# Optimization experiments

Measured on AMD Instinct MI355X. Metric: run time of the kernel, lower is better.

Reference implementation:

```python
import jax, jax.numpy as jnp
import numpy as np

N_NODES = 50000
N_EDGES = 800000
N_GRAPHS = 64
PIP = 3
N_CLASSES = 10
EPS = 1e-5


def setup_inputs() -> dict:
    key = jax.random.key(0)
    ks = jax.random.split(key, 32)
    s = 0.05
    d = {}
    d["node_feats"] = jax.random.normal(ks[0], (N_NODES, 128), jnp.float32)
    d["edge_w"] = jax.random.uniform(ks[1], (N_EDGES,), jnp.float32)
    # stacked per-branch params
    d["conv_w"] = jax.random.normal(ks[2], (PIP, 96, 128, 3), jnp.float32) * s
    d["conv_b"] = jax.random.normal(ks[3], (PIP, 96), jnp.float32) * s
    d["gcn_w"] = jax.random.normal(ks[4], (PIP, 96, 54), jnp.float32) * s
    d["gcn_b"] = jax.random.normal(ks[5], (PIP, 54), jnp.float32) * s
    d["bn1_g"] = jnp.ones((96,), jnp.float32)
    d["bn1_b"] = jnp.zeros((96,), jnp.float32)
    d["bn2_g"] = jnp.ones((54,), jnp.float32)
    d["bn2_b"] = jnp.zeros((54,), jnp.float32)
    d["bn3_g"] = jnp.ones((75,), jnp.float32)
    d["bn3_b"] = jnp.zeros((75,), jnp.float32)
    d["press_w"] = jax.random.normal(ks[6], (1, PIP, PIP), jnp.float32) * s
    d["press_b"] = jax.random.normal(ks[7], (1,), jnp.float32) * s
    d["jk_w1"] = jax.random.normal(ks[8], (54, 34), jnp.float32) * s
    d["jk_b1"] = jax.random.normal(ks[9], (34,), jnp.float32) * s
    d["jk_w2"] = jax.random.normal(ks[10], (34, 25), jnp.float32) * s
    d["jk_b2"] = jax.random.normal(ks[11], (25,), jnp.float32) * s
    d["jk_w3"] = jax.random.normal(ks[12], (25, 16), jnp.float32) * s
    d["jk_b3"] = jax.random.normal(ks[13], (16,), jnp.float32) * s
    d["cls1_w"] = jax.random.normal(ks[14], (75, 120), jnp.float32) * s
    d["cls1_b"] = jax.random.normal(ks[15], (120,), jnp.float32) * s
    d["cls2_w"] = jax.random.normal(ks[16], (120, N_CLASSES), jnp.float32) * s
    d["cls2_b"] = jax.random.normal(ks[17], (N_CLASSES,), jnp.float32) * s
    d["edge_src"] = jax.random.randint(ks[18], (N_EDGES,), 0, N_NODES)
    d["edge_dst"] = jax.random.randint(ks[19], (N_EDGES,), 0, N_NODES)
    d["graph_ids"] = jnp.sort(jax.random.randint(ks[20], (N_NODES,), 0, N_GRAPHS))
    return d


def _bn(x, g, b):
    # training-mode BatchNorm1d over axis 0
    m = x.mean(0)
    v = x.var(0)
    return g * (x - m) * jax.lax.rsqrt(v + EPS) + b


def _gconv(h, W, b, src, dst, ew, n):
    # DGL GraphConv norm='none': sum_{(u,v)} w_e * h[u] -> @W + b
    msg = h[src] * ew[:, None]              # [E, F]
    agg = jax.ops.segment_sum(msg, dst, num_segments=n)  # [N, F]
    return agg @ W + b


def _dconv1d(x, w, b, dil):
    # x: [1, Cin, N], w: [Cout, Cin, K]; 'same' length via pad=dil for K=3
    out = jax.lax.conv_general_dilated(
        x, w, window_strides=(1,), padding=[(dil, dil)],
        rhs_dilation=(dil,), dimension_numbers=('NCH', 'OIH', 'NCH'))
    return out + b[None, :, None]


def reference(node_feats, edge_w, conv_w, conv_b, gcn_w, gcn_b,
              bn1_g, bn1_b, bn2_g, bn2_b, bn3_g, bn3_b,
              press_w, press_b, jk_w1, jk_b1, jk_w2, jk_b2, jk_w3, jk_b3,
              cls1_w, cls1_b, cls2_w, cls2_b,
              edge_src, edge_dst, graph_ids):
    n = node_feats.shape[0]
    relu = jax.nn.relu
    # ---- BN_embedding ----
    h0 = node_feats.T[None]                # [1, 128, N]
    h0x = [_dconv1d(h0, conv_w[i], conv_b[i], i + 1) for i in range(PIP)]
    h2x = []
    for i in range(PIP):
        a = h0x[i % PIP][0].T              # [N, 96]
        c = h0x[(i + 1) % PIP][0].T        # [N, 96]
        h1 = _bn(relu(a) + c, bn1_g, bn1_b)          # cross_connect
        t = _gconv(h1, gcn_w[i], gcn_b[i], edge_src, edge_dst, edge_w, n)
        h2x.append(relu(t))                # [N, 54]
    stacked = jnp.stack(h2x, axis=1)       # [N, PIP, 54]
    pressed = jax.lax.conv_general_dilated(
        stacked, press_w, window_strides=(1,), padding='SAME',
        dimension_numbers=('NCH', 'OIH', 'NCH')) + press_b[None, :, None]
    emd_h = _bn(pressed[:, 0, :], bn2_g, bn2_b)      # [N, 54] (dropout = identity, eval)
    # ---- Presentation (JK readout) ----
    h1 = relu(_gconv(emd_h, jk_w1, jk_b1, edge_src, edge_dst, edge_w, n))
    h2 = relu(_gconv(h1, jk_w2, jk_b2, edge_src, edge_dst, edge_w, n))
    h3 = relu(_gconv(h2, jk_w3, jk_b3, edge_src, edge_dst, edge_w, n))
    ac_h = jnp.concatenate([h1, h2, h3], axis=1)     # [N, 75]
    hg = jax.ops.segment_sum(ac_h, graph_ids, num_segments=N_GRAPHS)  # [B, 75]
    logits = _bn(hg, bn3_g, bn3_b) @ cls1_w + cls1_b
    logits = logits @ cls2_w + cls2_b
    return (logits, emd_h)
```

## Files before the change

### kernel.cpp

```cpp
#include <hip/hip_runtime.h>
#include <hip/hip_bf16.h>

#define NND 50000
#define NED 800000
#define NGR 64
#define EPSV 1e-5f
#define NSTR (NND + 8)

__global__ void hist_kernel(const int* __restrict__ dst, int* __restrict__ cnt)
{
    int e = blockIdx.x * 256 + threadIdx.x;
    if (e < NED) atomicAdd(&cnt[dst[e]], 1);
}

__global__ void scanA_kernel(const int* __restrict__ cnt, int* __restrict__ bsum)
{
    __shared__ int buf[256];
    int t = threadIdx.x, base = blockIdx.x * 1024;
    int s = 0;
    for (int i = t; i < 1024; i += 256) {
        int idx = base + i;
        s += (idx < NND) ? cnt[idx] : 0;
    }
    buf[t] = s; __syncthreads();
    for (int off = 128; off; off >>= 1) {
        if (t < off) buf[t] += buf[t + off];
        __syncthreads();
    }
    if (t == 0) bsum[blockIdx.x] = buf[0];
}

__global__ void scanB_kernel(int* __restrict__ bsum, int* __restrict__ rowptr, int nb)
{
    if (threadIdx.x == 0) {
        int acc = 0;
        for (int i = 0; i < nb; i++) { int v = bsum[i]; bsum[i] = acc; acc += v; }
        rowptr[NND] = acc;
    }
}

__global__ void scanC_kernel(const int* __restrict__ cnt, const int* __restrict__ bsum,
                             int* __restrict__ rowptr, int* __restrict__ cursor)
{
    __shared__ int buf[1024];
    int t = threadIdx.x, idx = blockIdx.x * 1024 + t;
    int v = (idx < NND) ? cnt[idx] : 0;
    buf[t] = v; __syncthreads();
    for (int off = 1; off < 1024; off <<= 1) {
        int x = (t >= off) ? buf[t - off] : 0;
        __syncthreads();
        buf[t] += x;
        __syncthreads();
    }
    if (idx < NND) {
        int excl = buf[t] - v + bsum[blockIdx.x];
        rowptr[idx] = excl; cursor[idx] = excl;
    }
}

__global__ void fill_kernel(const int* __restrict__ src, const int* __restrict__ dst,
                            const float* __restrict__ ew, int* __restrict__ cursor,
                            int* __restrict__ csrs, float* __restrict__ csrw)
{
    int e = blockIdx.x * 256 + threadIdx.x;
    if (e < NED) {
        int pos = atomicAdd(&cursor[dst[e]], 1);
        csrs[pos] = src[e];
        csrw[pos] = ew[e];
    }
}

__global__ void grstart_kernel(const int* __restrict__ gid, int* __restrict__ gr)
{
    int t = threadIdx.x;
    if (t > NGR) return;
    if (t == NGR) { gr[NGR] = NND; return; }
    int lo = 0, hi = NND;
    while (lo < hi) { int mid = (lo + hi) >> 1; if (gid[mid] < t) lo = mid + 1; else hi = mid; }
    gr[t] = lo;
}

__global__ void transpose_kernel(const float* __restrict__ nf, float* __restrict__ nfT)
{
    __shared__ float tile[32][33];
    int tx = threadIdx.x & 31, ty = threadIdx.x >> 5;
    int p0 = blockIdx.x * 32, c0 = blockIdx.y * 32;
#pragma unroll
    for (int i = 0; i < 4; i++) {
        int p = p0 + ty + i * 8;
        if (p < NND) tile[ty + i * 8][tx] = nf[(size_t)p * 128 + c0 + tx];
    }
    __syncthreads();
#pragma unroll
    for (int i = 0; i < 4; i++) {
        int c = c0 + ty + i * 8;
        int p = p0 + tx;
        if (p < NND) nfT[(size_t)c * NSTR + 4 + p] = tile[tx][ty + i * 8];
    }
}

__global__ void pad_kernel(float* __restrict__ nfT)
{
    int t = threadIdx.x;
    int c = t >> 3, i = t & 7;
    size_t off = (size_t)c * NSTR + (i < 4 ? i : (NND + i));
    nfT[off] = 0.f;
}

template <int D>
__device__ __forceinline__ void conv_tap4(const float4& lo, const float4& mi, const float4& hi,
                                          const float* __restrict__ wl, int c,
                                          float (&acc)[4][4])
{
    float f0[4], f1[4], f2[4];
    f1[0] = mi.x; f1[1] = mi.y; f1[2] = mi.z; f1[3] = mi.w;
    if (D == 1) {
        f0[0] = lo.w; f0[1] = mi.x; f0[2] = mi.y; f0[3] = mi.z;
        f2[0] = mi.y; f2[1] = mi.z; f2[2] = mi.w; f2[3] = hi.x;
    } else if (D == 2) {
        f0[0] = lo.z; f0[1] = lo.w; f0[2] = mi.x; f0[3] = mi.y;
        f2[0] = mi.z; f2[1] = mi.w; f2[2] = hi.x; f2[3] = hi.y;
    } else {
        f0[0] = lo.y; f0[1] = lo.z; f0[2] = lo.w; f0[3] = mi.x;
        f2[0] = mi.w; f2[1] = hi.x; f2[2] = hi.y; f2[3] = hi.z;
    }
    const int BR = D - 1;
    const float4 a0 = *(const float4*)&wl[((BR * 3 + 0) * 128 + c) * 4];
    const float4 a1 = *(const float4*)&wl[((BR * 3 + 1) * 128 + c) * 4];
    const float4 a2 = *(const float4*)&wl[((BR * 3 + 2) * 128 + c) * 4];
#pragma unroll
    for (int i = 0; i < 4; i++) {
        acc[0][i] += f0[i] * a0.x + f1[i] * a1.x + f2[i] * a2.x;
        acc[1][i] += f0[i] * a0.y + f1[i] * a1.y + f2[i] * a2.y;
        acc[2][i] += f0[i] * a0.z + f1[i] * a1.z + f2[i] * a2.z;
        acc[3][i] += f0[i] * a0.w + f1[i] * a1.w + f2[i] * a2.w;
    }
}

__global__ __launch_bounds__(256)
void conv_y_stats_kernel(const float* __restrict__ nfT, const float* __restrict__ cw,
                         const float* __restrict__ cb, float* __restrict__ Y,
                         float* __restrict__ st1)
{
    __shared__ __align__(16) float wl[3 * 3 * 128 * 4];
    const int t  = threadIdx.x;
    const int og = blockIdx.x;
    for (int l = t; l < 3 * 3 * 128 * 4; l += 256) {
        int j = l & 3; int c = (l >> 2) & 127; int kb = l >> 9;
        int k = kb % 3, br = kb / 3;
        wl[l] = cw[(((size_t)br * 96 + og * 4 + j) * 128 + c) * 3 + k];
    }
    __syncthreads();
    const int pq = blockIdx.y * 1024 + t * 4;
    float acc[3][4][4];
#pragma unroll
    for (int br = 0; br < 3; br++)
#pragma unroll
        for (int j = 0; j < 4; j++) {
            float b = cb[br * 96 + og * 4 + j];
#pragma unroll
            for (int i = 0; i < 4; i++) acc[br][j][i] = b;
        }
    for (int c = 0; c < 128; c++) {
        const float* col = nfT + (size_t)c * NSTR + 4;
        float4 lo = *(const float4*)(col + pq - 4);
        float4 mi = *(const float4*)(col + pq);
        float4 hi = *(const float4*)(col + pq + 4);
        conv_tap4<1>(lo, mi, hi, wl, c, acc[0]);
        conv_tap4<2>(lo, mi, hi, wl, c, acc[1]);
        conv_tap4<3>(lo, mi, hi, wl, c, acc[2]);
    }
#pragma unroll
    for (int j = 0; j < 4; j++)
#pragma unroll
        for (int i = 0; i < 4; i++) {
            float a0 = acc[0][j][i], a1 = acc[1][j][i], a2 = acc[2][j][i];
            acc[0][j][i] = (a0 > 0.f ? a0 : 0.f) + a1;
            acc[1][j][i] = (a1 > 0.f ? a1 : 0.f) + a2;
            acc[2][j][i] = (a2 > 0.f ? a2 : 0.f) + a0;
        }
    bool val[4];
#pragma unroll
    for (int i = 0; i < 4; i++) val[i] = (pq + i) < NND;
    const size_t NM = (size_t)NND * 96;
#pragma unroll
    for (int br = 0; br < 3; br++)
#pragma unroll
        for (int j = 0; j < 4; j++) {
            float s = 0.f, q = 0.f;
#pragma unroll
            for (int i = 0; i < 4; i++)
                if (val[i]) { float v = acc[br][j][i]; s += v; q += v * v; }
            for (int off = 32; off; off >>= 1) {
                s += __shfl_down(s, off, 64);
                q += __shfl_down(q, off, 64);
            }
            if ((t & 63) == 0) {
                unsafeAtomicAdd(&st1[br * 96 + og * 4 + j], s);
                unsafeAtomicAdd(&st1[288 + br * 96 + og * 4 + j], q);
            }
        }
#pragma unroll
    for (int br = 0; br < 3; br++)
#pragma unroll
        for (int i = 0; i < 4; i++) {
            if (!val[i]) continue;
            float* yo = Y + (size_t)br * NM + (size_t)(pq + i) * 96 + og * 4;
            float4 v;
            v.x = acc[br][0][i]; v.y = acc[br][1][i]; v.z = acc[br][2][i]; v.w = acc[br][3][i];
            *(float4*)yo = v;
        }
}

__global__ void bn_finalize_kernel(const float* __restrict__ st, const float* __restrict__ g,
                                   const float* __restrict__ b,
                                   float* __restrict__ sc, float* __restrict__ sh,
                                   int C, int gmod)
{
    int t = threadIdx.x;
    if (t >= C) return;
    float mean = st[t] / (float)NND;
    float var  = st[C + t] / (float)NND - mean * mean;
    float rs = rsqrtf(var + EPSV);
    float gg = g[t % gmod], bb = b[t % gmod];
    float s = gg * rs;
    sc[t] = s; sh[t] = bb - mean * s;
}

__global__ void pull_bn_kernel(const float* __restrict__ Y, const int* __restrict__ rowptr,
                               const int* __restrict__ csrs, const float* __restrict__ csrw,
                               const float* __restrict__ sc1, const float* __restrict__ sh1,
                               float* __restrict__ AGG)
{
    int id = blockIdx.x * 256 + threadIdx.x;
    if (id >= NND * 24) return;
    int p = id / 24, q = id % 24;
    const float4* Y4 = (const float4*)Y;
    const size_t NQ = (size_t)NND * 24;
    int beg = rowptr[p], end = rowptr[p + 1];
    float a0x=0,a0y=0,a0z=0,a0w=0, a1x=0,a1y=0,a1z=0,a1w=0, a2x=0,a2y=0,a2z=0,a2w=0;
    float wsum = 0.f;
    for (int i = beg; i < end; i++) {
        float w = csrw[i];
        size_t off = (size_t)csrs[i] * 24 + q;
        float4 v0 = Y4[off];
        float4 v1 = Y4[NQ + off];
        float4 v2 = Y4[2 * NQ + off];
        a0x += w * v0.x; a0y += w * v0.y; a0z += w * v0.z; a0w += w * v0.w;
        a1x += w * v1.x; a1y += w * v1.y; a1z += w * v1.z; a1w += w * v1.w;
        a2x += w * v2.x; a2y += w * v2.y; a2z += w * v2.z; a2w += w * v2.w;
        wsum += w;
    }
    const float4* S4 = (const float4*)sc1;
    const float4* H4 = (const float4*)sh1;
    float4* AG4 = (float4*)AGG;
    size_t ob = (size_t)p * 24 + q;
    {
        float4 s = S4[q], h = H4[q], r;
        r.x = s.x * a0x + h.x * wsum; r.y = s.y * a0y + h.y * wsum;
        r.z = s.z * a0z + h.z * wsum; r.w = s.w * a0w + h.w * wsum;
        AG4[ob] = r;
    }
    {
        float4 s = S4[24 + q], h = H4[24 + q], r;
        r.x = s.x * a1x + h.x * wsum; r.y = s.y * a1y + h.y * wsum;
        r.z = s.z * a1z + h.z * wsum; r.w = s.w * a1w + h.w * wsum;
        AG4[NQ + ob] = r;
    }
    {
        float4 s = S4[48 + q], h = H4[48 + q], r;
        r.x = s.x * a2x + h.x * wsum; r.y = s.y * a2y + h.y * wsum;
        r.z = s.z * a2z + h.z * wsum; r.w = s.w * a2w + h.w * wsum;
        AG4[2 * NQ + ob] = r;
    }
}

template <int C>
__global__ void pull2_kernel(const float* __restrict__ in, const int* __restrict__ rowptr,
                             const int* __restrict__ csrs, const float* __restrict__ csrw,
                             float* __restrict__ out)
{
    constexpr int C2 = C / 2;
    int id = blockIdx.x * 256 + threadIdx.x;
    if (id >= NND * C2) return;
    int p = id / C2, q = id % C2;
    const float2* in2 = (const float2*)in;
    int beg = rowptr[p], end = rowptr[p + 1];
    float ax = 0.f, ay = 0.f;
    for (int i = beg; i < end; i++) {
        float w = csrw[i];
        float2 v = in2[(size_t)csrs[i] * C2 + q];
        ax += w * v.x; ay += w * v.y;
    }
    float2 r; r.x = ax; r.y = ay;
    ((float2*)out)[(size_t)p * C2 + q] = r;
}

template <int C>
__global__ void pull_kernel(const float* __restrict__ in, const int* __restrict__ rowptr,
                            const int* __restrict__ csrs, const float* __restrict__ csrw,
                            float* __restrict__ out)
{
    int id = blockIdx.x * 256 + threadIdx.x;
    if (id >= NND * C) return;
    int p = id / C, c = id % C;
    int beg = rowptr[p], end = rowptr[p + 1];
    float acc = 0.f;
    for (int i = beg; i < end; i++)
        acc += csrw[i] * in[(size_t)csrs[i] * C + c];
    out[id] = acc;
}

template <int Cin, int Cout>
__global__ __launch_bounds__(128)
void matmul_node_kernel(const float* __restrict__ in, const float* __restrict__ W,
                        const float* __restrict__ bias, float* __restrict__ out)
{
    constexpr int CoutP = (Cout + 3) & ~3;
    __shared__ __align__(16) float wl[Cin * CoutP];
    __shared__ float bl[CoutP];
    const int t = threadIdx.x;
    const int br = blockIdx.y;
    const float* Wb = W + (size_t)br * Cin * Cout;
    for (int l = t; l < Cin * CoutP; l += 128) {
        int c = l / CoutP, o = l % CoutP;
        wl[l] = (o < Cout) ? Wb[c * Cout + o] : 0.f;
    }
    if (t < CoutP) bl[t] = (t < Cout) ? bias[br * Cout + t] : 0.f;
    __syncthreads();
    int p = blockIdx.x * 128 + t;
    if (p >= NND) return;
    float acc[CoutP];
#pragma unroll
    for (int o = 0; o < CoutP; o++) acc[o] = bl[o];
    const float* row = in + (size_t)br * NND * Cin + (size_t)p * Cin;
    if constexpr (Cin % 4 == 0) {
        const float4* row4 = (const float4*)row;
#pragma unroll
        for (int c4 = 0; c4 < Cin / 4; c4++) {
            float4 f4 = row4[c4];
            float fv[4] = {f4.x, f4.y, f4.z, f4.w};
#pragma unroll
            for (int cc = 0; cc < 4; cc++) {
                const float4* w4 = (const float4*)&wl[(c4 * 4 + cc) * CoutP];
#pragma unroll
                for (int oq = 0; oq < CoutP / 4; oq++) {
                    float4 wv = w4[oq];
                    acc[oq * 4 + 0] += fv[cc] * wv.x;
                    acc[oq * 4 + 1] += fv[cc] * wv.y;
                    acc[oq * 4 + 2] += fv[cc] * wv.z;
                    acc[oq * 4 + 3] += fv[cc] * wv.w;
                }
            }
        }
    } else if constexpr (Cin % 2 == 0) {
        const float2* row2 = (const float2*)row;
#pragma unroll
        for (int c2 = 0; c2 < Cin / 2; c2++) {
            float2 f2 = row2[c2];
            float fv[2] = {f2.x, f2.y};
#pragma unroll
            for (int cc = 0; cc < 2; cc++) {
                const float4* w4 = (const float4*)&wl[(c2 * 2 + cc) * CoutP];
#pragma unroll
                for (int oq = 0; oq < CoutP / 4; oq++) {
                    float4 wv = w4[oq];
                    acc[oq * 4 + 0] += fv[cc] * wv.x;
                    acc[oq * 4 + 1] += fv[cc] * wv.y;
                    acc[oq * 4 + 2] += fv[cc] * wv.z;
                    acc[oq * 4 + 3] += fv[cc] * wv.w;
                }
            }
        }
    } else {
#pragma unroll
        for (int c = 0; c < Cin; c++) {
            float f = row[c];
            const float4* w4 = (const float4*)&wl[c * CoutP];
#pragma unroll
            for (int oq = 0; oq < CoutP / 4; oq++) {
                float4 wv = w4[oq];
                acc[oq * 4 + 0] += f * wv.x;
                acc[oq * 4 + 1] += f * wv.y;
                acc[oq * 4 + 2] += f * wv.z;
                acc[oq * 4 + 3] += f * wv.w;
            }
        }
    }
    float* op = out + (size_t)br * NND * Cout + (size_t)p * Cout;
    if constexpr (Cout % 2 == 0) {
#pragma unroll
        for (int o2 = 0; o2 < Cout / 2; o2++) {
            float2 r;
            r.x = acc[o2 * 2] > 0.f ? acc[o2 * 2] : 0.f;
            r.y = acc[o2 * 2 + 1] > 0.f ? acc[o2 * 2 + 1] : 0.f;
            ((float2*)op)[o2] = r;
        }
    } else {
#pragma unroll
        for (int o = 0; o < Cout; o++) op[o] = acc[o] > 0.f ? acc[o] : 0.f;
    }
}

__global__ void press_stats_kernel(const float* __restrict__ H2, const float* __restrict__ pw,
                                   const float* __restrict__ pb, float* __restrict__ PRS,
                                   float* __restrict__ st2)
{
    __shared__ float ls[54], lq[54];
    int t = threadIdx.x;
    if (t < 54) { ls[t] = 0.f; lq[t] = 0.f; }
    __syncthreads();
    float pwf[9];
#pragma unroll
    for (int q = 0; q < 9; q++) pwf[q] = pw[q];
    float pbf = pb[0];
    const size_t NM = (size_t)NND * 54;
    size_t base = (size_t)blockIdx.x * 6912;
    for (int q = 0; q < 27; q++) {
        size_t idx = base + q * 256 + t;
        if (idx < NM) {
            int p = (int)(idx / 54), h = (int)(idx % 54);
            float sum = pbf;
#pragma unroll
            for (int i = 0; i < 3; i++)
#pragma unroll
                for (int k = 0; k < 3; k++) {
                    int hh = h + k - 1;
                    if (hh >= 0 && hh < 54)
                        sum += pwf[i * 3 + k] * H2[(size_t)i * NM + (size_t)p * 54 + hh];
                }
            PRS[idx] = sum;
            atomicAdd(&ls[h], sum); atomicAdd(&lq[h], sum * sum);
        }
    }
    __syncthreads();
    if (t < 54) {
        unsafeAtomicAdd(&st2[t], ls[t]);
        unsafeAtomicAdd(&st2[54 + t], lq[t]);
    }
}

__global__ void emd_kernel(float* __restrict__ PRS, const float* __restrict__ sc2,
                           const float* __restrict__ sh2, float* __restrict__ outp)
{
    int id = blockIdx.x * 256 + threadIdx.x;
    if (id >= NND * 54) return;
    int h = id % 54;
    float v = PRS[id] * sc2[h] + sh2[h];
    PRS[id] = v;
    outp[id] = v;
}

__global__ void pool_kernel(const float* __restrict__ H1, const float* __restrict__ H2j,
                            const float* __restrict__ H3, const int* __restrict__ gr,
                            float* __restrict__ HG)
{
    __shared__ float part[4][75];
    int t = threadIdx.x;
    int c = t % 75, sub = t / 75;
    int g = blockIdx.x;
    int s = gr[g], e = gr[g + 1];
    float acc = 0.f;
    for (int p = s + sub; p < e; p += 4) {
        float v;
        if (c < 34)      v = H1[(size_t)p * 34 + c];
        else if (c < 59) v = H2j[(size_t)p * 25 + (c - 34)];
        else             v = H3[(size_t)p * 16 + (c - 59)];
        acc += v;
    }
    part[sub][c] = acc;
    __syncthreads();
    if (t < 75) HG[g * 75 + t] = part[0][t] + part[1][t] + part[2][t] + part[3][t];
}

__global__ void final_kernel(const float* __restrict__ HG, const float* __restrict__ g3,
                             const float* __restrict__ b3,
                             const float* __restrict__ w1, const float* __restrict__ b1,
                             const float* __restrict__ w2, const float* __restrict__ b2,
                             float* __restrict__ outp)
{
    __shared__ float hg[64 * 75];
    __shared__ float o1[64 * 120];
    __shared__ float sc[75], sh[75];
    int t = threadIdx.x;
    for (int idx = t; idx < 64 * 75; idx += 512) hg[idx] = HG[idx];
    __syncthreads();
    if (t < 75) {
        float s = 0.f, q = 0.f;
        for (int r = 0; r < 64; r++) { float v = hg[r * 75 + t]; s += v; q += v * v; }
        float m = s / 64.f, var = q / 64.f - m * m;
        float rs = rsqrtf(var + EPSV);
        float scale = g3[t] * rs;
        sc[t] = scale; sh[t] = b3[t] - m * scale;
    }
    __syncthreads();
    for (int idx = t; idx < 64 * 75; idx += 512) { int c = idx % 75; hg[idx] = hg[idx] * sc[c] + sh[c]; }
    __syncthreads();
    for (int idx = t; idx < 64 * 120; idx += 512) {
        int r = idx / 120, o = idx % 120;
        float a = b1[o];
        for (int c = 0; c < 75; c++) a += hg[r * 75 + c] * w1[c * 120 + o];
        o1[idx] = a;
    }
    __syncthreads();
    for (int idx = t; idx < 640; idx += 512) {
        int r = idx / 10, o = idx % 10;
        float a = b2[o];
        for (int k = 0; k < 120; k++) a += o1[r * 120 + k] * w2[k * 10 + o];
        outp[idx] = a;
    }
}

extern "C" void kernel_launch(void* const* d_in, const int* in_sizes, int n_in,
                              void* d_out, int out_size, void* d_ws, size_t ws_size,
                              hipStream_t stream)
{
    (void)in_sizes; (void)n_in; (void)out_size;
    const float* nf     = (const float*)d_in[0];
    const float* ew     = (const float*)d_in[1];
    const float* conv_w = (const float*)d_in[2];
    const float* conv_b = (const float*)d_in[3];
    const float* gcn_w  = (const float*)d_in[4];
    const float* gcn_b  = (const float*)d_in[5];
    const float* bn1_g = (const float*)d_in[6],  *bn1_b = (const float*)d_in[7];
    const float* bn2_g = (const float*)d_in[8],  *bn2_b = (const float*)d_in[9];
    const float* bn3_g = (const float*)d_in[10], *bn3_b = (const float*)d_in[11];
    const float* press_w = (const float*)d_in[12], *press_b = (const float*)d_in[13];
    const float* jk_w1 = (const float*)d_in[14], *jk_b1 = (const float*)d_in[15];
    const float* jk_w2 = (const float*)d_in[16], *jk_b2 = (const float*)d_in[17];
    const float* jk_w3 = (const float*)d_in[18], *jk_b3 = (const float*)d_in[19];
    const float* cls1_w = (const float*)d_in[20], *cls1_b = (const float*)d_in[21];
    const float* cls2_w = (const float*)d_in[22], *cls2_b = (const float*)d_in[23];
    const int* esrc = (const int*)d_in[24];
    const int* edst = (const int*)d_in[25];
    const int* gid  = (const int*)d_in[26];
    float* out = (float*)d_out;

    float* ws = (float*)d_ws;
    const size_t NM = (size_t)NND * 96;
    const size_t N54 = (size_t)NND * 54;
    float* X   = ws;
    float* Y   = X + 3 * NM;
    float* H2c = Y + 3 * NM;
    float* PRS = H2c + 3 * N54;
    float* ST1 = PRS + N54;
    float* SC1 = ST1 + 576;
    float* SH1 = SC1 + 288;
    float* ST2 = SH1 + 288;
    float* SC2 = ST2 + 108;
    float* SH2 = SC2 + 54;
    float* HG  = SH2 + 54;
    int* CNT    = (int*)(HG + 4800);
    int* ROWPTR = CNT + NND;
    int* CURSOR = ROWPTR + NND + 1;
    int* CSRS   = CURSOR + NND;
    float* CSRW = (float*)(CSRS + NED);
    int* BSUM   = (int*)(CSRW + NED);
    int* GR     = BSUM + 64;
    size_t need = (size_t)((float*)(GR + 65) - ws) * sizeof(float);
    if (ws_size < need) return;

    float* nfT  = X;
    float* AGG  = X;
    float* AGG1 = Y;
    float* H1j  = AGG1 + N54;
    float* AGG2 = H1j + (size_t)NND * 34;
    float* H2j  = AGG2 + (size_t)NND * 34;
    float* AGG3 = H2j + (size_t)NND * 25;
    float* H3j  = AGG3 + (size_t)NND * 25;

    hipMemsetAsync(ST1, 0, 1368 * sizeof(float), stream);
    hipMemsetAsync(CNT, 0, NND * sizeof(int), stream);

    hist_kernel<<<(NED + 255) / 256, 256, 0, stream>>>(edst, CNT);
    scanA_kernel<<<49, 256, 0, stream>>>(CNT, BSUM);
    scanB_kernel<<<1, 64, 0, stream>>>(BSUM, ROWPTR, 49);
    scanC_kernel<<<49, 1024, 0, stream>>>(CNT, BSUM, ROWPTR, CURSOR);
    fill_kernel<<<(NED + 255) / 256, 256, 0, stream>>>(esrc, edst, ew, CURSOR, CSRS, CSRW);
    grstart_kernel<<<1, 128, 0, stream>>>(gid, GR);

    transpose_kernel<<<dim3((NND + 31) / 32, 4), 256, 0, stream>>>(nf, nfT);
    pad_kernel<<<1, 1024, 0, stream>>>(nfT);

    conv_y_stats_kernel<<<dim3(24, 49), 256, 0, stream>>>(nfT, conv_w, conv_b, Y, ST1);
    bn_finalize_kernel<<<1, 512, 0, stream>>>(ST1, bn1_g, bn1_b, SC1, SH1, 288, 96);

    pull_bn_kernel<<<(NND * 24 + 255) / 256, 256, 0, stream>>>(
        Y, ROWPTR, CSRS, CSRW, SC1, SH1, AGG);

    matmul_node_kernel<96, 54><<<dim3((NND + 127) / 128, 3), 128, 0, stream>>>(
        AGG, gcn_w, gcn_b, H2c);

    press_stats_kernel<<<(int)((N54 + 6911) / 6912), 256, 0, stream>>>(H2c, press_w, press_b, PRS, ST2);
    bn_finalize_kernel<<<1, 512, 0, stream>>>(ST2, bn2_g, bn2_b, SC2, SH2, 54, 54);
    emd_kernel<<<(int)((N54 + 255) / 256), 256, 0, stream>>>(PRS, SC2, SH2, out + 640);

    pull2_kernel<54><<<(NND * 27 + 255) / 256, 256, 0, stream>>>(PRS, ROWPTR, CSRS, CSRW, AGG1);
    matmul_node_kernel<54, 34><<<dim3((NND + 127) / 128, 1), 128, 0, stream>>>(
        AGG1, jk_w1, jk_b1, H1j);

    pull2_kernel<34><<<(NND * 17 + 255) / 256, 256, 0, stream>>>(H1j, ROWPTR, CSRS, CSRW, AGG2);
    matmul_node_kernel<34, 25><<<dim3((NND + 127) / 128, 1), 128, 0, stream>>>(
        AGG2, jk_w2, jk_b2, H2j);

    pull_kernel<25><<<(NND * 25 + 255) / 256, 256, 0, stream>>>(H2j, ROWPTR, CSRS, CSRW, AGG3);
    matmul_node_kernel<25, 16><<<dim3((NND + 127) / 128, 1), 128, 0, stream>>>(
        AGG3, jk_w3, jk_b3, H3j);

    pool_kernel<<<NGR, 300, 0, stream>>>(H1j, H2j, H3j, GR, HG);
    final_kernel<<<1, 512, 0, stream>>>(HG, bn3_g, bn3_b, cls1_w, cls1_b, cls2_w, cls2_b, out);
}
```

Measured before the change: 988.8 us.

## Reorder GraphConv to transform-then-aggregate and fold BN into GCN weights

Every GraphConv now runs the node-wise matmul before the sparse aggregation, so the gather works on the narrower output width (54/34/25/16 instead of 96/54/34/25). The first layer's BatchNorm scale and shift are folded into the GCN weights and a bias by a small kernel. Bias and ReLU move into the pull kernels. This cuts gathered bytes per edge, and the shift-times-weight-sum term becomes a folded bias that goes through aggregation. It changes floating-point summation order.

```diff
diff --git a/kernel.cpp b/kernel.cpp
--- a/kernel.cpp
+++ b/kernel.cpp
@@ -227,58 +227,156 @@
     sc[t] = s; sh[t] = bb - mean * s;
 }
 
-__global__ void pull_bn_kernel(const float* __restrict__ Y, const int* __restrict__ rowptr,
-                               const int* __restrict__ csrs, const float* __restrict__ csrw,
-                               const float* __restrict__ sc1, const float* __restrict__ sh1,
-                               float* __restrict__ AGG)
+__global__ void fold_w_kernel(const float* __restrict__ gw, const float* __restrict__ sc1,
+                              const float* __restrict__ sh1,
+                              float* __restrict__ WP, float* __restrict__ BP)
+{
+    int t = blockIdx.x * 256 + threadIdx.x;
+    if (t >= 3 * 54) return;
+    int br = t / 54, o = t % 54;
+    const float* W = gw + (size_t)br * 96 * 54 + o;
+    float bacc = 0.f;
+    for (int c = 0; c < 96; c++) {
+        float w = W[c * 54];
+        WP[((size_t)br * 96 + c) * 54 + o] = sc1[br * 96 + c] * w;
+        bacc += sh1[br * 96 + c] * w;
+    }
+    BP[br * 54 + o] = bacc;
+}
+
+template <int Cin, int Cout, bool RELU>
+__global__ __launch_bounds__(128)
+void matmul_node_kernel(const float* __restrict__ in, const float* __restrict__ W,
+                        const float* __restrict__ bias, float* __restrict__ out)
+{
+    constexpr int CoutP = (Cout + 3) & ~3;
+    __shared__ __align__(16) float wl[Cin * CoutP];
+    __shared__ float bl[CoutP];
+    const int t = threadIdx.x;
+    const int br = blockIdx.y;
+    const float* Wb = W + (size_t)br * Cin * Cout;
+    for (int l = t; l < Cin * CoutP; l += 128) {
+        int c = l / CoutP, o = l % CoutP;
+        wl[l] = (o < Cout) ? Wb[c * Cout + o] : 0.f;
+    }
+    if (t < CoutP) bl[t] = (t < Cout && bias) ? bias[br * Cout + t] : 0.f;
+    __syncthreads();
+    int p = blockIdx.x * 128 + t;
+    if (p >= NND) return;
+    float acc[CoutP];
+#pragma unroll
+    for (int o = 0; o < CoutP; o++) acc[o] = bl[o];
+    const float* row = in + (size_t)br * NND * Cin + (size_t)p * Cin;
+    if constexpr (Cin % 4 == 0) {
+        const float4* row4 = (const float4*)row;
+#pragma unroll
+        for (int c4 = 0; c4 < Cin / 4; c4++) {
+            float4 f4 = row4[c4];
+            float fv[4] = {f4.x, f4.y, f4.z, f4.w};
+#pragma unroll
+            for (int cc = 0; cc < 4; cc++) {
+                const float4* w4 = (const float4*)&wl[(c4 * 4 + cc) * CoutP];
+#pragma unroll
+                for (int oq = 0; oq < CoutP / 4; oq++) {
+                    float4 wv = w4[oq];
+                    acc[oq * 4 + 0] += fv[cc] * wv.x;
+                    acc[oq * 4 + 1] += fv[cc] * wv.y;
+                    acc[oq * 4 + 2] += fv[cc] * wv.z;
+                    acc[oq * 4 + 3] += fv[cc] * wv.w;
+                }
+            }
+        }
+    } else if constexpr (Cin % 2 == 0) {
+        const float2* row2 = (const float2*)row;
+#pragma unroll
+        for (int c2 = 0; c2 < Cin / 2; c2++) {
+            float2 f2 = row2[c2];
+            float fv[2] = {f2.x, f2.y};
+#pragma unroll
+            for (int cc = 0; cc < 2; cc++) {
+                const float4* w4 = (const float4*)&wl[(c2 * 2 + cc) * CoutP];
+#pragma unroll
+                for (int oq = 0; oq < CoutP / 4; oq++) {
+                    float4 wv = w4[oq];
+                    acc[oq * 4 + 0] += fv[cc] * wv.x;
+                    acc[oq * 4 + 1] += fv[cc] * wv.y;
+                    acc[oq * 4 + 2] += fv[cc] * wv.z;
+                    acc[oq * 4 + 3] += fv[cc] * wv.w;
+                }
+            }
+        }
+    } else {
+#pragma unroll
+        for (int c = 0; c < Cin; c++) {
+            float f = row[c];
+            const float4* w4 = (const float4*)&wl[c * CoutP];
+#pragma unroll
+            for (int oq = 0; oq < CoutP / 4; oq++) {
+                float4 wv = w4[oq];
+                acc[oq * 4 + 0] += f * wv.x;
+                acc[oq * 4 + 1] += f * wv.y;
+                acc[oq * 4 + 2] += f * wv.z;
+                acc[oq * 4 + 3] += f * wv.w;
+            }
+        }
+    }
+    float* op = out + (size_t)br * NND * Cout + (size_t)p * Cout;
+#pragma unroll
+    for (int o = 0; o < Cout; o++) {
+        float v = acc[o];
+        if constexpr (RELU) v = v > 0.f ? v : 0.f;
+        op[o] = v;
+    }
+}
+
+__global__ void pull3br54_kernel(const float* __restrict__ Z, const int* __restrict__ rowptr,
+                                 const int* __restrict__ csrs, const float* __restrict__ csrw,
+                                 const float* __restrict__ gb, float* __restrict__ H2c)
 {
     int id = blockIdx.x * 256 + threadIdx.x;
-    if (id >= NND * 24) return;
-    int p = id / 24, q = id % 24;
-    const float4* Y4 = (const float4*)Y;
-    const size_t NQ = (size_t)NND * 24;
+    if (id >= NND * 27) return;
+    int p = id / 27, q = id % 27;
+    const float2* Z2 = (const float2*)Z;
+    const size_t NQ = (size_t)NND * 27;
     int beg = rowptr[p], end = rowptr[p + 1];
-    float a0x=0,a0y=0,a0z=0,a0w=0, a1x=0,a1y=0,a1z=0,a1w=0, a2x=0,a2y=0,a2z=0,a2w=0;
-    float wsum = 0.f;
+    float a0x=0,a0y=0, a1x=0,a1y=0, a2x=0,a2y=0;
     for (int i = beg; i < end; i++) {
         float w = csrw[i];
-        size_t off = (size_t)csrs[i] * 24 + q;
-        float4 v0 = Y4[off];
-        float4 v1 = Y4[NQ + off];
-        float4 v2 = Y4[2 * NQ + off];
-        a0x += w * v0.x; a0y += w * v0.y; a0z += w * v0.z; a0w += w * v0.w;
-        a1x += w * v1.x; a1y += w * v1.y; a1z += w * v1.z; a1w += w * v1.w;
-        a2x += w * v2.x; a2y += w * v2.y; a2z += w * v2.z; a2w += w * v2.w;
-        wsum += w;
-    }
-    const float4* S4 = (const float4*)sc1;
-    const float4* H4 = (const float4*)sh1;
-    float4* AG4 = (float4*)AGG;
-    size_t ob = (size_t)p * 24 + q;
+        size_t off = (size_t)csrs[i] * 27 + q;
+        float2 v0 = Z2[off];
+        float2 v1 = Z2[NQ + off];
+        float2 v2 = Z2[2 * NQ + off];
+        a0x += w * v0.x; a0y += w * v0.y;
+        a1x += w * v1.x; a1y += w * v1.y;
+        a2x += w * v2.x; a2y += w * v2.y;
+    }
+    const float2* GB2 = (const float2*)gb;
+    float2* O2 = (float2*)H2c;
+    size_t ob = (size_t)p * 27 + q;
     {
-        float4 s = S4[q], h = H4[q], r;
-        r.x = s.x * a0x + h.x * wsum; r.y = s.y * a0y + h.y * wsum;
-        r.z = s.z * a0z + h.z * wsum; r.w = s.w * a0w + h.w * wsum;
-        AG4[ob] = r;
+        float2 b = GB2[q], r;
+        r.x = a0x + b.x; r.y = a0y + b.y;
+        r.x = r.x > 0.f ? r.x : 0.f; r.y = r.y > 0.f ? r.y : 0.f;
+        O2[ob] = r;
     }
     {
-        float4 s = S4[24 + q], h = H4[24 + q], r;
-        r.x = s.x * a1x + h.x * wsum; r.y = s.y * a1y + h.y * wsum;
-        r.z = s.z * a1z + h.z * wsum; r.w = s.w * a1w + h.w * wsum;
-        AG4[NQ + ob] = r;
+        float2 b = GB2[27 + q], r;
+        r.x = a1x + b.x; r.y = a1y + b.y;
+        r.x = r.x > 0.f ? r.x : 0.f; r.y = r.y > 0.f ? r.y : 0.f;
+        O2[NQ + ob] = r;
     }
     {
-        float4 s = S4[48 + q], h = H4[48 + q], r;
-        r.x = s.x * a2x + h.x * wsum; r.y = s.y * a2y + h.y * wsum;
-        r.z = s.z * a2z + h.z * wsum; r.w = s.w * a2w + h.w * wsum;
-        AG4[2 * NQ + ob] = r;
+        float2 b = GB2[54 + q], r;
+        r.x = a2x + b.x; r.y = a2y + b.y;
+        r.x = r.x > 0.f ? r.x : 0.f; r.y = r.y > 0.f ? r.y : 0.f;
+        O2[2 * NQ + ob] = r;
     }
 }
 
 template <int C>
-__global__ void pull2_kernel(const float* __restrict__ in, const int* __restrict__ rowptr,
-                             const int* __restrict__ csrs, const float* __restrict__ csrw,
-                             float* __restrict__ out)
+__global__ void pull_br2_kernel(const float* __restrict__ in, const int* __restrict__ rowptr,
+                                const int* __restrict__ csrs, const float* __restrict__ csrw,
+                                const float* __restrict__ bias, float* __restrict__ out)
 {
     constexpr int C2 = C / 2;
     int id = blockIdx.x * 256 + threadIdx.x;
@@ -292,14 +390,17 @@
         float2 v = in2[(size_t)csrs[i] * C2 + q];
         ax += w * v.x; ay += w * v.y;
     }
-    float2 r; r.x = ax; r.y = ay;
+    float2 b = ((const float2*)bias)[q];
+    float2 r;
+    r.x = ax + b.x; r.y = ay + b.y;
+    r.x = r.x > 0.f ? r.x : 0.f; r.y = r.y > 0.f ? r.y : 0.f;
     ((float2*)out)[(size_t)p * C2 + q] = r;
 }
 
 template <int C>
-__global__ void pull_kernel(const float* __restrict__ in, const int* __restrict__ rowptr,
-                            const int* __restrict__ csrs, const float* __restrict__ csrw,
-                            float* __restrict__ out)
+__global__ void pull_br1_kernel(const float* __restrict__ in, const int* __restrict__ rowptr,
+                                const int* __restrict__ csrs, const float* __restrict__ csrw,
+                                const float* __restrict__ bias, float* __restrict__ out)
 {
     int id = blockIdx.x * 256 + threadIdx.x;
     if (id >= NND * C) return;
@@ -308,98 +409,33 @@
     float acc = 0.f;
     for (int i = beg; i < end; i++)
         acc += csrw[i] * in[(size_t)csrs[i] * C + c];
-    out[id] = acc;
-}
-
-template <int Cin, int Cout>
-__global__ __launch_bounds__(128)
-void matmul_node_kernel(const float* __restrict__ in, const float* __restrict__ W,
-                        const float* __restrict__ bias, float* __restrict__ out)
-{
-    constexpr int CoutP = (Cout + 3) & ~3;
-    __shared__ __align__(16) float wl[Cin * CoutP];
-    __shared__ float bl[CoutP];
-    const int t = threadIdx.x;
-    const int br = blockIdx.y;
-    const float* Wb = W + (size_t)br * Cin * Cout;
-    for (int l = t; l < Cin * CoutP; l += 128) {
-        int c = l / CoutP, o = l % CoutP;
-        wl[l] = (o < Cout) ? Wb[c * Cout + o] : 0.f;
-    }
-    if (t < CoutP) bl[t] = (t < Cout) ? bias[br * Cout + t] : 0.f;
-    __syncthreads();
-    int p = blockIdx.x * 128 + t;
-    if (p >= NND) return;
-    float acc[CoutP];
-#pragma unroll
-    for (int o = 0; o < CoutP; o++) acc[o] = bl[o];
-    const float* row = in + (size_t)br * NND * Cin + (size_t)p * Cin;
-    if constexpr (Cin % 4 == 0) {
-        const float4* row4 = (const float4*)row;
-#pragma unroll
-        for (int c4 = 0; c4 < Cin / 4; c4++) {
-            float4 f4 = row4[c4];
-            float fv[4] = {f4.x, f4.y, f4.z, f4.w};
-#pragma unroll
-            for (int cc = 0; cc < 4; cc++) {
-                const float4* w4 = (const float4*)&wl[(c4 * 4 + cc) * CoutP];
-#pragma unroll
-                for (int oq = 0; oq < CoutP / 4; oq++) {
-                    float4 wv = w4[oq];
-                    acc[oq * 4 + 0] += fv[cc] * wv.x;
-                    acc[oq * 4 + 1] += fv[cc] * wv.y;
-                    acc[oq * 4 + 2] += fv[cc] * wv.z;
-                    acc[oq * 4 + 3] += fv[cc] * wv.w;
-                }
-            }
-        }
-    } else if constexpr (Cin % 2 == 0) {
-        const float2* row2 = (const float2*)row;
-#pragma unroll
-        for (int c2 = 0; c2 < Cin / 2; c2++) {
-            float2 f2 = row2[c2];
-            float fv[2] = {f2.x, f2.y};
-#pragma unroll
-            for (int cc = 0; cc < 2; cc++) {
-                const float4* w4 = (const float4*)&wl[(c2 * 2 + cc) * CoutP];
-#pragma unroll
-                for (int oq = 0; oq < CoutP / 4; oq++) {
-                    float4 wv = w4[oq];
-                    acc[oq * 4 + 0] += fv[cc] * wv.x;
-                    acc[oq * 4 + 1] += fv[cc] * wv.y;
-                    acc[oq * 4 + 2] += fv[cc] * wv.z;
-                    acc[oq * 4 + 3] += fv[cc] * wv.w;
-                }
-            }
-        }
-    } else {
-#pragma unroll
-        for (int c = 0; c < Cin; c++) {
-            float f = row[c];
-            const float4* w4 = (const float4*)&wl[c * CoutP];
-#pragma unroll
-            for (int oq = 0; oq < CoutP / 4; oq++) {
-                float4 wv = w4[oq];
-                acc[oq * 4 + 0] += f * wv.x;
-                acc[oq * 4 + 1] += f * wv.y;
-                acc[oq * 4 + 2] += f * wv.z;
-                acc[oq * 4 + 3] += f * wv.w;
-            }
-        }
-    }
-    float* op = out + (size_t)br * NND * Cout + (size_t)p * Cout;
-    if constexpr (Cout % 2 == 0) {
-#pragma unroll
-        for (int o2 = 0; o2 < Cout / 2; o2++) {
-            float2 r;
-            r.x = acc[o2 * 2] > 0.f ? acc[o2 * 2] : 0.f;
-            r.y = acc[o2 * 2 + 1] > 0.f ? acc[o2 * 2 + 1] : 0.f;
-            ((float2*)op)[o2] = r;
-        }
-    } else {
-#pragma unroll
-        for (int o = 0; o < Cout; o++) op[o] = acc[o] > 0.f ? acc[o] : 0.f;
-    }
+    float v = acc + bias[c];
+    out[id] = v > 0.f ? v : 0.f;
+}
+
+template <int C>
+__global__ void pull_br4_kernel(const float* __restrict__ in, const int* __restrict__ rowptr,
+                                const int* __restrict__ csrs, const float* __restrict__ csrw,
+                                const float* __restrict__ bias, float* __restrict__ out)
+{
+    constexpr int C4 = C / 4;
+    int id = blockIdx.x * 256 + threadIdx.x;
+    if (id >= NND * C4) return;
+    int p = id / C4, q = id % C4;
+    const float4* in4 = (const float4*)in;
+    int beg = rowptr[p], end = rowptr[p + 1];
+    float ax = 0.f, ay = 0.f, az = 0.f, aw = 0.f;
+    for (int i = beg; i < end; i++) {
+        float w = csrw[i];
+        float4 v = in4[(size_t)csrs[i] * C4 + q];
+        ax += w * v.x; ay += w * v.y; az += w * v.z; aw += w * v.w;
+    }
+    float4 b = ((const float4*)bias)[q];
+    float4 r;
+    r.x = ax + b.x; r.y = ay + b.y; r.z = az + b.z; r.w = aw + b.w;
+    r.x = r.x > 0.f ? r.x : 0.f; r.y = r.y > 0.f ? r.y : 0.f;
+    r.z = r.z > 0.f ? r.z : 0.f; r.w = r.w > 0.f ? r.w : 0.f;
+    ((float4*)out)[(size_t)p * C4 + q] = r;
 }
 
 __global__ void press_stats_kernel(const float* __restrict__ H2, const float* __restrict__ pw,
@@ -557,17 +593,19 @@
     float* CSRW = (float*)(CSRS + NED);
     int* BSUM   = (int*)(CSRW + NED);
     int* GR     = BSUM + 64;
-    size_t need = (size_t)((float*)(GR + 65) - ws) * sizeof(float);
+    float* WP   = (float*)(GR + 68);
+    float* BP   = WP + 15552;
+    size_t need = (size_t)((BP + 162) - ws) * sizeof(float);
     if (ws_size < need) return;
 
     float* nfT  = X;
-    float* AGG  = X;
-    float* AGG1 = Y;
-    float* H1j  = AGG1 + N54;
-    float* AGG2 = H1j + (size_t)NND * 34;
-    float* H2j  = AGG2 + (size_t)NND * 34;
-    float* AGG3 = H2j + (size_t)NND * 25;
-    float* H3j  = AGG3 + (size_t)NND * 25;
+    float* Z    = X;
+    float* P1   = Y;
+    float* H1j  = P1 + (size_t)NND * 34;
+    float* P2   = H1j + (size_t)NND * 34;
+    float* H2j  = P2 + (size_t)NND * 25;
+    float* P3   = H2j + (size_t)NND * 25;
+    float* H3j  = P3 + (size_t)NND * 16;
 
     hipMemsetAsync(ST1, 0, 1368 * sizeof(float), stream);
     hipMemsetAsync(CNT, 0, NND * sizeof(int), stream);
@@ -585,27 +623,31 @@
     conv_y_stats_kernel<<<dim3(24, 49), 256, 0, stream>>>(nfT, conv_w, conv_b, Y, ST1);
     bn_finalize_kernel<<<1, 512, 0, stream>>>(ST1, bn1_g, bn1_b, SC1, SH1, 288, 96);
 
-    pull_bn_kernel<<<(NND * 24 + 255) / 256, 256, 0, stream>>>(
-        Y, ROWPTR, CSRS, CSRW, SC1, SH1, AGG);
-
-    matmul_node_kernel<96, 54><<<dim3((NND + 127) / 128, 3), 128, 0, stream>>>(
-        AGG, gcn_w, gcn_b, H2c);
+    fold_w_kernel<<<1, 256, 0, stream>>>(gcn_w, SC1, SH1, WP, BP);
+    matmul_node_kernel<96, 54, false><<<dim3((NND + 127) / 128, 3), 128, 0, stream>>>(
+        Y, WP, BP, Z);
+
+    pull3br54_kernel<<<(NND * 27 + 255) / 256, 256, 0, stream>>>(
+        Z, ROWPTR, CSRS, CSRW, gcn_b, H2c);
 
     press_stats_kernel<<<(int)((N54 + 6911) / 6912), 256, 0, stream>>>(H2c, press_w, press_b, PRS, ST2);
     bn_finalize_kernel<<<1, 512, 0, stream>>>(ST2, bn2_g, bn2_b, SC2, SH2, 54, 54);
     emd_kernel<<<(int)((N54 + 255) / 256), 256, 0, stream>>>(PRS, SC2, SH2, out + 640);
 
-    pull2_kernel<54><<<(NND * 27 + 255) / 256, 256, 0, stream>>>(PRS, ROWPTR, CSRS, CSRW, AGG1);
-    matmul_node_kernel<54, 34><<<dim3((NND + 127) / 128, 1), 128, 0, stream>>>(
-        AGG1, jk_w1, jk_b1, H1j);
-
-    pull2_kernel<34><<<(NND * 17 + 255) / 256, 256, 0, stream>>>(H1j, ROWPTR, CSRS, CSRW, AGG2);
-    matmul_node_kernel<34, 25><<<dim3((NND + 127) / 128, 1), 128, 0, stream>>>(
-        AGG2, jk_w2, jk_b2, H2j);
-
-    pull_kernel<25><<<(NND * 25 + 255) / 256, 256, 0, stream>>>(H2j, ROWPTR, CSRS, CSRW, AGG3);
-    matmul_node_kernel<25, 16><<<dim3((NND + 127) / 128, 1), 128, 0, stream>>>(
-        AGG3, jk_w3, jk_b3, H3j);
+    matmul_node_kernel<54, 34, false><<<dim3((NND + 127) / 128, 1), 128, 0, stream>>>(
+        PRS, jk_w1, nullptr, P1);
+    pull_br2_kernel<34><<<(NND * 17 + 255) / 256, 256, 0, stream>>>(
+        P1, ROWPTR, CSRS, CSRW, jk_b1, H1j);
+
+    matmul_node_kernel<34, 25, false><<<dim3((NND + 127) / 128, 1), 128, 0, stream>>>(
+        H1j, jk_w2, nullptr, P2);
+    pull_br1_kernel<25><<<(NND * 25 + 255) / 256, 256, 0, stream>>>(
+        P2, ROWPTR, CSRS, CSRW, jk_b2, H2j);
+
+    matmul_node_kernel<25, 16, false><<<dim3((NND + 127) / 128, 1), 128, 0, stream>>>(
+        H2j, jk_w3, nullptr, P3);
+    pull_br4_kernel<16><<<(NND * 4 + 255) / 256, 256, 0, stream>>>(
+        P3, ROWPTR, CSRS, CSRW, jk_b3, H3j);
 
     pool_kernel<<<NGR, 300, 0, stream>>>(H1j, H2j, H3j, GR, HG);
     final_kernel<<<1, 512, 0, stream>>>(HG, bn3_g, bn3_b, cls1_w, cls1_b, cls2_w, cls2_b, out);
```

After: 939.2 us. -5.0%, faster.
